# Kernel optimization log

Measured on AMD Instinct MI355X. Metric: run time of the kernel, lower is better.

The kernel has to match this reference:

```python
import jax, jax.numpy as jnp
import numpy as np

D_MODEL = 256
NUM_HEADS = 8
DIM_HEAD = D_MODEL // NUM_HEADS
EPS = 1e-6
MASK_BIAS = -1.0e9


def setup_inputs() -> dict:
    key = jax.random.key(0)
    ks = jax.random.split(key, 10)
    B, S = 2, 4096
    x = jax.random.normal(ks[0], (B, S, D_MODEL), dtype=jnp.float32)
    pad_mask = jnp.zeros((B, S), dtype=jnp.float32)  # 1.0 => padded position
    scale = 1.0 / np.sqrt(D_MODEL)
    Wq = jax.random.normal(ks[1], (D_MODEL, D_MODEL), dtype=jnp.float32) * scale
    bq = jnp.zeros((D_MODEL,), dtype=jnp.float32)
    Wk = jax.random.normal(ks[2], (D_MODEL, D_MODEL), dtype=jnp.float32) * scale
    bk = jnp.zeros((D_MODEL,), dtype=jnp.float32)
    Wv = jax.random.normal(ks[3], (D_MODEL, D_MODEL), dtype=jnp.float32) * scale
    bv = jnp.zeros((D_MODEL,), dtype=jnp.float32)
    gamma = jnp.ones((D_MODEL,), dtype=jnp.float32)
    beta = jnp.zeros((D_MODEL,), dtype=jnp.float32)
    return {"x": x, "pad_mask": pad_mask, "Wq": Wq, "bq": bq, "Wk": Wk,
            "bk": bk, "Wv": Wv, "bv": bv, "gamma": gamma, "beta": beta}


def _layer_norm(h, gamma, beta):
    mu = jnp.mean(h, axis=-1, keepdims=True)
    var = jnp.mean(jnp.square(h - mu), axis=-1, keepdims=True)
    return gamma * (h - mu) * jax.lax.rsqrt(var + EPS) + beta


def reference(x, pad_mask, Wq, bq, Wk, bk, Wv, bv, gamma, beta):
    B, S, D = x.shape
    q = x @ Wq + bq  # [B,S,D]
    k = x @ Wk + bk
    v = x @ Wv + bv
    # split heads: [B,S,D] -> [B,H,S,Dh]
    def split(t):
        return t.reshape(B, S, NUM_HEADS, DIM_HEAD).transpose(0, 2, 1, 3)
    qh, kh, vh = split(q), split(k), split(v)
    w = jnp.einsum("bhqd,bhkd->bhqk", qh, kh)  # [B,H,S,S]
    # faithful to source: mask added BEFORE the 1/sqrt(dim_head) scaling
    w = w + pad_mask[:, None, None, :] * MASK_BIAS
    w = w / jnp.sqrt(jnp.float32(DIM_HEAD))
    attn = jax.nn.softmax(w, axis=-1)
    # dropout is identity at inference
    out = jnp.einsum("bhqk,bhkd->bhqd", attn, vh)  # [B,H,S,Dh]
    out = out.transpose(0, 2, 1, 3).reshape(B, S, D)
    return _layer_norm(out + x, gamma, beta)
```

## Files before the change

kernel.cpp:

```cpp
#include <hip/hip_runtime.h>
#include <hip/hip_bf16.h>

#define D_MODEL 256
#define NUM_HEADS 8
#define DIM_HEAD 32
#define SEQ 4096
#define BATCH 2
#define NROWS (BATCH * SEQ)
#define LN_EPS 1e-6f
#define MASK_BIAS -1.0e9f
#define SCALE 0.17677669529663687f
#define LOG2E 1.4426950408889634f
#define QSCALE (SCALE * LOG2E)

typedef __attribute__((ext_vector_type(8))) short short8;
typedef __attribute__((ext_vector_type(4))) float f32x4;

static __device__ __forceinline__ unsigned short f2b(float f) {
    union { __hip_bfloat16 b; unsigned short u; } cv;
    cv.b = __float2bfloat16(f);
    return cv.u;
}
static __device__ __forceinline__ unsigned int pk_bf16(float lo, float hi) {
    union { __hip_bfloat162 v; unsigned int u; } cv;
    cv.v = __float22bfloat162_rn(make_float2(lo, hi));
    return cv.u;
}
static __device__ __forceinline__ float exp2_raw(float x) {
#if __has_builtin(__builtin_amdgcn_exp2f)
    return __builtin_amdgcn_exp2f(x);
#else
    float r;
    asm volatile("v_exp_f32 %0, %1" : "=v"(r) : "v"(x));
    return r;
#endif
}
static __device__ __forceinline__ void load_lds16(const void* g, void* l) {
    __builtin_amdgcn_global_load_lds(
        (const __attribute__((address_space(1))) unsigned int*)g,
        (__attribute__((address_space(3))) unsigned int*)l, 16, 0, 0);
}

__global__ __launch_bounds__(256) void prep_kernel(
    const float* __restrict__ Wq, const float* __restrict__ Wk,
    const float* __restrict__ Wv,
    const float* __restrict__ bq, const float* __restrict__ bk,
    const float* __restrict__ bv,
    const float* __restrict__ pad,
    unsigned short* __restrict__ Wt, float* __restrict__ biasc,
    float* __restrict__ T2)
{
    const int blk = blockIdx.x;
    const int t = threadIdx.x;
    if (blk < 48) {
        const int w = blk >> 4;
        const int k0 = (blk & 15) * 16;
        const float* W = (w == 0) ? Wq : (w == 1) ? Wk : Wv;
        float v[16];
        #pragma unroll
        for (int k = 0; k < 16; k++)
            v[k] = W[(size_t)(k0 + k) * 256 + t];
        unsigned int u[8];
        #pragma unroll
        for (int i = 0; i < 8; i++)
            u[i] = pk_bf16(v[2 * i], v[2 * i + 1]);
        unsigned short* dst = Wt + (size_t)(w * 256 + t) * 256 + k0;
        *(uint4*)(dst)     = make_uint4(u[0], u[1], u[2], u[3]);
        *(uint4*)(dst + 8) = make_uint4(u[4], u[5], u[6], u[7]);
        if ((blk & 15) == 0) {
            const float* bb = (w == 0) ? bq : (w == 1) ? bk : bv;
            biasc[w * 256 + t] = bb[t];
        }
    } else {
        const int i = (blk - 48) * 256 + t;
        T2[i] = pad[i] * (MASK_BIAS * SCALE * LOG2E);
    }
}

__global__ __launch_bounds__(256) void qkv_mfma_kernel(
    const float* __restrict__ x, const unsigned short* __restrict__ Wt,
    const float* __restrict__ biasc,
    unsigned short* __restrict__ Qh, unsigned short* __restrict__ Kh,
    unsigned short* __restrict__ Vt)
{
    __shared__ float LW[4][16][102];

    const int lane = threadIdx.x & 63;
    const int wid  = threadIdx.x >> 6;
    const int c    = lane & 15;
    const int quad = lane >> 4;

    const int r0 = (blockIdx.x >> 3) * 64 + wid * 16;
    const int n0 = (blockIdx.x & 7) * 96;

    f32x4 acc[6];
    float bias[6];
    #pragma unroll
    for (int t = 0; t < 6; t++) {
        acc[t] = (f32x4){0.f, 0.f, 0.f, 0.f};
        bias[t] = biasc[n0 + 16 * t + c];
    }

    const float* xp0 = x + (size_t)(r0 + c) * D_MODEL + quad * 8;
    const unsigned short* wp0 = Wt + (size_t)(n0 + c) * 256 + quad * 8;

    for (int k0 = 0; k0 < 256; k0 += 32) {
        const float4 a0 = *(const float4*)(xp0 + k0);
        const float4 a1 = *(const float4*)(xp0 + k0 + 4);
        union { unsigned int u[4]; short8 s; } af;
        af.u[0] = pk_bf16(a0.x, a0.y);
        af.u[1] = pk_bf16(a0.z, a0.w);
        af.u[2] = pk_bf16(a1.x, a1.y);
        af.u[3] = pk_bf16(a1.z, a1.w);
        #pragma unroll
        for (int t = 0; t < 6; t++) {
            const short8 bf = *(const short8*)(wp0 + (size_t)(16 * t) * 256 + k0);
            acc[t] = __builtin_amdgcn_mfma_f32_16x16x32_bf16(af.s, bf, acc[t], 0, 0, 0);
        }
    }

    float* lw = &LW[wid][0][0];
    #pragma unroll
    for (int t = 0; t < 6; t++) {
        const int col = n0 + 16 * t;
        const int mm  = col >> 8;
        float v0 = acc[t][0] + bias[t];
        float v1 = acc[t][1] + bias[t];
        float v2 = acc[t][2] + bias[t];
        float v3 = acc[t][3] + bias[t];
        if (mm == 2) {
            const int dim = (col & 255) + c;
            const int h = dim >> 5, d = dim & 31;
            const int row = r0 + quad * 4;
            const int bb = row >> 12;
            const int s  = row & (SEQ - 1);
            const size_t bh = (size_t)(bb * NUM_HEADS + h);
            uint2 pk = make_uint2(pk_bf16(v0, v1), pk_bf16(v2, v3));
            *(uint2*)(Vt + (bh * DIM_HEAD + d) * SEQ + s) = pk;
        } else {
            if (mm == 0) {
                v0 *= QSCALE; v1 *= QSCALE; v2 *= QSCALE; v3 *= QSCALE;
            }
            const int e = 16 * t + c;
            lw[(quad * 4 + 0) * 102 + e] = v0;
            lw[(quad * 4 + 1) * 102 + e] = v1;
            lw[(quad * 4 + 2) * 102 + e] = v2;
            lw[(quad * 4 + 3) * 102 + e] = v3;
        }
    }

    #pragma unroll
    for (int hg = 0; hg < 3; hg++) {
        const int col32 = n0 + 32 * hg;
        const int mm = col32 >> 8;
        if (mm == 2) continue;
        unsigned short* Pm = (mm == 0) ? Qh : Kh;
        const int h = (col32 & 255) >> 5;
        const int row = r0 + (lane & 15);
        const size_t bh = (size_t)((row >> 12) * NUM_HEADS + h);
        const int srow = row & (SEQ - 1);
        unsigned short* Pr = Pm + (bh * SEQ + srow) * DIM_HEAD;
        #pragma unroll
        for (int ii = 0; ii < 2; ii++) {
            const int cc = (lane >> 4) + 4 * ii;
            const int e = (lane & 15) * 102 + 32 * hg + cc * 4;
            const float2 lo = *(const float2*)&lw[e];
            const float2 hi = *(const float2*)&lw[e + 2];
            uint2 pk = make_uint2(pk_bf16(lo.x, lo.y), pk_bf16(hi.x, hi.y));
            *(uint2*)(Pr + cc * 4) = pk;
        }
    }
}

__global__ __launch_bounds__(512, 4) void attn_mfma_kernel(
    const unsigned short* __restrict__ Qh, const unsigned short* __restrict__ Kh,
    const unsigned short* __restrict__ Vt, const float* __restrict__ T2,
    float* __restrict__ O)
{
    __shared__ __align__(16) unsigned char smem[50688];
    unsigned short* smem_s = (unsigned short*)smem;
    float* Tf = (float*)(smem + 49152);

    const int lane = threadIdx.x & 63;
    const int wid  = threadIdx.x >> 6;
    const int cwid = wid & 3;
    const int shalf = wid >> 2;
    const int c    = lane & 15;
    const int quad = lane >> 4;

    const int gw = blockIdx.x;
    const int q0 = (gw & 31) * 128;
    const int h  = (gw >> 5) & (NUM_HEADS - 1);
    const int b  = gw >> 8;
    const size_t bh = (size_t)(b * NUM_HEADS + h);

    const int perm = ((c & 12) << 1) | (c & 3);

    const unsigned short* Kb = Kh + bh * SEQ * DIM_HEAD;
    const unsigned short* Vb = Vt + bh * DIM_HEAD * SEQ;
    const float* Tb = T2 + (size_t)b * SEQ;

    const int qrow = q0 + cwid * 32;
    const short8 qfA = *(const short8*)(Qh + (bh * SEQ + qrow + c) * DIM_HEAD + quad * 8);
    const short8 qfB = *(const short8*)(Qh + (bh * SEQ + qrow + 16 + c) * DIM_HEAD + quad * 8);

    union { unsigned int u[4]; short8 s; } ones;
    ones.u[0] = ones.u[1] = ones.u[2] = ones.u[3] = 0x3F803F80u;

    const int f0 = ((perm >> 1) ^ (perm >> 3)) & 3;
    const int f1 = (((perm + 4) >> 1) ^ ((perm + 4) >> 3)) & 3;
    const int kA = perm * 32 + ((quad ^ f0) << 3);
    const int kB = (perm + 4) * 32 + ((quad ^ f1) << 3);
    const int g0 = quad ^ (c & 7);
    const int vbase0 = c * 128 + (g0 << 3);
    const int vbase1 = (16 + c) * 128 + (g0 << 3);

    const int skey = (lane >> 2);
    const int sgK  = lane & 3;
    const int sdim = lane >> 4;
    const int sgV  = lane & 15;

    f32x4 oA0 = {0.f,0.f,0.f,0.f}, oA1 = {0.f,0.f,0.f,0.f};
    f32x4 oB0 = {0.f,0.f,0.f,0.f}, oB1 = {0.f,0.f,0.f,0.f};
    f32x4 laccA = {0.f,0.f,0.f,0.f}, laccB = {0.f,0.f,0.f,0.f};

    auto stage = [&](int ch, int pb) {
        const int s0 = ch * 128;
        if (wid < 4) {
            #pragma unroll
            for (int jj = 0; jj < 2; jj++) {
                const int j = wid * 2 + jj;
                const int key = j * 16 + skey;
                const int f = ((key >> 1) ^ (key >> 3)) & 3;
                load_lds16(Kb + (size_t)(s0 + key) * 32 + ((sgK ^ f) << 3),
                           &smem_s[pb * 4096 + j * 512]);
            }
        } else {
            #pragma unroll
            for (int jj = 0; jj < 2; jj++) {
                const int j = (wid - 4) * 2 + jj;
                const int dim = j * 4 + sdim;
                load_lds16(Vb + (size_t)dim * SEQ + s0 + ((sgV ^ (dim & 7)) << 3),
                           &smem_s[12288 + pb * 4096 + j * 512]);
            }
            if (wid == 7 && lane < 32)
                load_lds16(Tb + s0 + lane * 4, Tf + pb * 128);
        }
    };

    auto sub = [&](int pb, int s) {
        const short8 kf0 = *(const short8*)&smem_s[pb * 4096 + s * 1024 + kA];
        const short8 kf1 = *(const short8*)&smem_s[pb * 4096 + s * 1024 + kB];
        const short8 vf0 = *(const short8*)&smem_s[12288 + pb * 4096 + (vbase0 ^ (s << 5))];
        const short8 vf1 = *(const short8*)&smem_s[12288 + pb * 4096 + (vbase1 ^ (s << 5))];
        const f32x4 c0 = *(const f32x4*)&Tf[pb * 128 + s * 32 + quad * 8];
        const f32x4 c1 = *(const f32x4*)&Tf[pb * 128 + s * 32 + quad * 8 + 4];

        const f32x4 sA0 = __builtin_amdgcn_mfma_f32_16x16x32_bf16(kf0, qfA, c0, 0, 0, 0);
        const f32x4 sA1 = __builtin_amdgcn_mfma_f32_16x16x32_bf16(kf1, qfA, c1, 0, 0, 0);
        const f32x4 sB0 = __builtin_amdgcn_mfma_f32_16x16x32_bf16(kf0, qfB, c0, 0, 0, 0);
        const f32x4 sB1 = __builtin_amdgcn_mfma_f32_16x16x32_bf16(kf1, qfB, c1, 0, 0, 0);

        union { unsigned int u[4]; short8 s8; } pfA, pfB;
        {
            float p0 = exp2_raw(sA0[0]), p1 = exp2_raw(sA0[1]);
            float p2 = exp2_raw(sA0[2]), p3 = exp2_raw(sA0[3]);
            float p4 = exp2_raw(sA1[0]), p5 = exp2_raw(sA1[1]);
            float p6 = exp2_raw(sA1[2]), p7 = exp2_raw(sA1[3]);
            pfA.u[0] = pk_bf16(p0, p1);
            pfA.u[1] = pk_bf16(p2, p3);
            pfA.u[2] = pk_bf16(p4, p5);
            pfA.u[3] = pk_bf16(p6, p7);
        }
        {
            float p0 = exp2_raw(sB0[0]), p1 = exp2_raw(sB0[1]);
            float p2 = exp2_raw(sB0[2]), p3 = exp2_raw(sB0[3]);
            float p4 = exp2_raw(sB1[0]), p5 = exp2_raw(sB1[1]);
            float p6 = exp2_raw(sB1[2]), p7 = exp2_raw(sB1[3]);
            pfB.u[0] = pk_bf16(p0, p1);
            pfB.u[1] = pk_bf16(p2, p3);
            pfB.u[2] = pk_bf16(p4, p5);
            pfB.u[3] = pk_bf16(p6, p7);
        }

        laccA = __builtin_amdgcn_mfma_f32_16x16x32_bf16(ones.s, pfA.s8, laccA, 0, 0, 0);
        laccB = __builtin_amdgcn_mfma_f32_16x16x32_bf16(ones.s, pfB.s8, laccB, 0, 0, 0);
        oA0   = __builtin_amdgcn_mfma_f32_16x16x32_bf16(vf0,   pfA.s8, oA0,   0, 0, 0);
        oA1   = __builtin_amdgcn_mfma_f32_16x16x32_bf16(vf1,   pfA.s8, oA1,   0, 0, 0);
        oB0   = __builtin_amdgcn_mfma_f32_16x16x32_bf16(vf0,   pfB.s8, oB0,   0, 0, 0);
        oB1   = __builtin_amdgcn_mfma_f32_16x16x32_bf16(vf1,   pfB.s8, oB1,   0, 0, 0);
    };

    stage(0, 0);
    stage(1, 1);

    int rb = 0;
    int sb = 2;
    for (int ch = 0; ch < SEQ / 128; ++ch) {
        if (wid == 7)
            asm volatile("s_waitcnt vmcnt(3) lgkmcnt(0)" ::: "memory");
        else
            asm volatile("s_waitcnt vmcnt(2) lgkmcnt(0)" ::: "memory");
        __builtin_amdgcn_s_barrier();
        __builtin_amdgcn_sched_barrier(0);
        stage((ch + 2) & 31, sb);
        sub(rb, shalf * 2);
        sub(rb, shalf * 2 + 1);
        rb = (rb == 2) ? 0 : rb + 1;
        sb = (sb == 2) ? 0 : sb + 1;
    }

    asm volatile("s_waitcnt vmcnt(0) lgkmcnt(0)" ::: "memory");
    __builtin_amdgcn_s_barrier();

    float* CS = (float*)smem;
    if (wid >= 4) {
        const int slot = ((cwid * 64) + lane) * 20;
        *(f32x4*)&CS[slot + 0]  = oA0;
        *(f32x4*)&CS[slot + 4]  = oA1;
        *(f32x4*)&CS[slot + 8]  = oB0;
        *(f32x4*)&CS[slot + 12] = oB1;
        CS[slot + 16] = laccA[0];
        CS[slot + 17] = laccB[0];
    }
    asm volatile("s_waitcnt lgkmcnt(0)" ::: "memory");
    __builtin_amdgcn_s_barrier();
    if (wid < 4) {
        const int slot = ((cwid * 64) + lane) * 20;
        const f32x4 pA0 = *(const f32x4*)&CS[slot + 0];
        const f32x4 pA1 = *(const f32x4*)&CS[slot + 4];
        const f32x4 pB0 = *(const f32x4*)&CS[slot + 8];
        const f32x4 pB1 = *(const f32x4*)&CS[slot + 12];
        const float invA = 1.0f / (laccA[0] + CS[slot + 16]);
        const float invB = 1.0f / (laccB[0] + CS[slot + 17]);
        oA0 += pA0; oA1 += pA1; oB0 += pB0; oB1 += pB1;

        float* opA = O + ((size_t)(b * SEQ) + qrow + c) * D_MODEL + h * DIM_HEAD + quad * 4;
        float* opB = O + ((size_t)(b * SEQ) + qrow + 16 + c) * D_MODEL + h * DIM_HEAD + quad * 4;
        *(float4*)opA        = make_float4(oA0[0]*invA, oA0[1]*invA, oA0[2]*invA, oA0[3]*invA);
        *(float4*)(opA + 16) = make_float4(oA1[0]*invA, oA1[1]*invA, oA1[2]*invA, oA1[3]*invA);
        *(float4*)opB        = make_float4(oB0[0]*invB, oB0[1]*invB, oB0[2]*invB, oB0[3]*invB);
        *(float4*)(opB + 16) = make_float4(oB1[0]*invB, oB1[1]*invB, oB1[2]*invB, oB1[3]*invB);
    }
}

__global__ __launch_bounds__(256) void ln_kernel(
    float* AO,
    const float* __restrict__ x,
    const float* __restrict__ gamma, const float* __restrict__ beta)
{
    const int lane = threadIdx.x & 63;
    const int wid  = threadIdx.x >> 6;
    const size_t row = (size_t)blockIdx.x * 4 + wid;

    const float4 a  = ((const float4*)(AO + row * D_MODEL))[lane];
    const float4 xv = ((const float4*)(x + row * D_MODEL))[lane];
    float hv[4];
    hv[0] = a.x + xv.x;
    hv[1] = a.y + xv.y;
    hv[2] = a.z + xv.z;
    hv[3] = a.w + xv.w;

    float s = hv[0] + hv[1] + hv[2] + hv[3];
    #pragma unroll
    for (int off = 32; off > 0; off >>= 1) s += __shfl_xor(s, off, 64);
    const float mu = s * (1.0f / D_MODEL);

    float d0 = hv[0]-mu, d1 = hv[1]-mu, d2 = hv[2]-mu, d3 = hv[3]-mu;
    float ss = d0*d0 + d1*d1 + d2*d2 + d3*d3;
    #pragma unroll
    for (int off = 32; off > 0; off >>= 1) ss += __shfl_xor(ss, off, 64);
    const float rs = rsqrtf(ss * (1.0f / D_MODEL) + LN_EPS);

    const float4 g  = ((const float4*)gamma)[lane];
    const float4 bb = ((const float4*)beta)[lane];
    float4 y;
    y.x = g.x * d0 * rs + bb.x;
    y.y = g.y * d1 * rs + bb.y;
    y.z = g.z * d2 * rs + bb.z;
    y.w = g.w * d3 * rs + bb.w;
    ((float4*)(AO + row * D_MODEL))[lane] = y;
}

extern "C" void kernel_launch(void* const* d_in, const int* in_sizes, int n_in,
                              void* d_out, int out_size, void* d_ws, size_t ws_size,
                              hipStream_t stream)
{
    const float* x     = (const float*)d_in[0];
    const float* pad   = (const float*)d_in[1];
    const float* Wq    = (const float*)d_in[2];
    const float* bq    = (const float*)d_in[3];
    const float* Wk    = (const float*)d_in[4];
    const float* bk    = (const float*)d_in[5];
    const float* Wv    = (const float*)d_in[6];
    const float* bv    = (const float*)d_in[7];
    const float* gamma = (const float*)d_in[8];
    const float* beta  = (const float*)d_in[9];

    const size_t elems = (size_t)NROWS * D_MODEL;
    unsigned short* Qh = (unsigned short*)d_ws;
    unsigned short* Kh = Qh + elems;
    unsigned short* Vt = Kh + elems;
    float* T2 = (float*)(Vt + elems);
    unsigned short* Wt = (unsigned short*)(T2 + NROWS);
    float* biasc = (float*)(Wt + 768 * 256);
    float* AO = (float*)d_out;

    prep_kernel<<<80, 256, 0, stream>>>(Wq, Wk, Wv, bq, bk, bv, pad,
                                        Wt, biasc, T2);
    qkv_mfma_kernel<<<(NROWS / 64) * 8, 256, 0, stream>>>(x, Wt, biasc,
                                                          Qh, Kh, Vt);
    attn_mfma_kernel<<<BATCH * NUM_HEADS * (SEQ / 128), 512, 0, stream>>>(
        Qh, Kh, Vt, T2, AO);
    ln_kernel<<<NROWS / 4, 256, 0, stream>>>(AO, x, gamma, beta);
}
```

Measured before the change: 171.8 us.

## Software-pipeline PV MFMAs one chunk behind QK and exp computation

Splits the per-chunk attention step into a QK+exp stage and a PV accumulation stage. The PV MFMAs for the previous chunk are issued in the current iteration, using probabilities and V fragments held in registers. The aim is to overlap MFMA work with the exp2/packing VALU work and hide the dependency between exp and PV. The cost is extra register pressure from carrying eight short8 values across iterations, a prologue and an epilogue, and more sched_barriers.

```diff
diff --git a/kernel.cpp b/kernel.cpp
--- a/kernel.cpp
+++ b/kernel.cpp
@@ -224,6 +224,9 @@
     f32x4 oB0 = {0.f,0.f,0.f,0.f}, oB1 = {0.f,0.f,0.f,0.f};
     f32x4 laccA = {0.f,0.f,0.f,0.f}, laccB = {0.f,0.f,0.f,0.f};
 
+    short8 d_pfA0, d_pfB0, d_vf00, d_vf01;
+    short8 d_pfA1, d_pfB1, d_vf10, d_vf11;
+
     auto stage = [&](int ch, int pb) {
         const int s0 = ch * 128;
         if (wid < 4) {
@@ -248,11 +251,12 @@
         }
     };
 
-    auto sub = [&](int pb, int s) {
+    auto subQK = [&](int pb, int s, short8& o_pfA, short8& o_pfB,
+                     short8& o_vf0, short8& o_vf1) {
         const short8 kf0 = *(const short8*)&smem_s[pb * 4096 + s * 1024 + kA];
         const short8 kf1 = *(const short8*)&smem_s[pb * 4096 + s * 1024 + kB];
-        const short8 vf0 = *(const short8*)&smem_s[12288 + pb * 4096 + (vbase0 ^ (s << 5))];
-        const short8 vf1 = *(const short8*)&smem_s[12288 + pb * 4096 + (vbase1 ^ (s << 5))];
+        o_vf0 = *(const short8*)&smem_s[12288 + pb * 4096 + (vbase0 ^ (s << 5))];
+        o_vf1 = *(const short8*)&smem_s[12288 + pb * 4096 + (vbase1 ^ (s << 5))];
         const f32x4 c0 = *(const f32x4*)&Tf[pb * 128 + s * 32 + quad * 8];
         const f32x4 c1 = *(const f32x4*)&Tf[pb * 128 + s * 32 + quad * 8 + 4];
 
@@ -282,21 +286,42 @@
             pfB.u[2] = pk_bf16(p4, p5);
             pfB.u[3] = pk_bf16(p6, p7);
         }
-
-        laccA = __builtin_amdgcn_mfma_f32_16x16x32_bf16(ones.s, pfA.s8, laccA, 0, 0, 0);
-        laccB = __builtin_amdgcn_mfma_f32_16x16x32_bf16(ones.s, pfB.s8, laccB, 0, 0, 0);
-        oA0   = __builtin_amdgcn_mfma_f32_16x16x32_bf16(vf0,   pfA.s8, oA0,   0, 0, 0);
-        oA1   = __builtin_amdgcn_mfma_f32_16x16x32_bf16(vf1,   pfA.s8, oA1,   0, 0, 0);
-        oB0   = __builtin_amdgcn_mfma_f32_16x16x32_bf16(vf0,   pfB.s8, oB0,   0, 0, 0);
-        oB1   = __builtin_amdgcn_mfma_f32_16x16x32_bf16(vf1,   pfB.s8, oB1,   0, 0, 0);
+        o_pfA = pfA.s8;
+        o_pfB = pfB.s8;
+    };
+
+    auto PV = [&]() {
+        laccA = __builtin_amdgcn_mfma_f32_16x16x32_bf16(ones.s, d_pfA0, laccA, 0, 0, 0);
+        laccB = __builtin_amdgcn_mfma_f32_16x16x32_bf16(ones.s, d_pfB0, laccB, 0, 0, 0);
+        oA0   = __builtin_amdgcn_mfma_f32_16x16x32_bf16(d_vf00, d_pfA0, oA0,   0, 0, 0);
+        oA1   = __builtin_amdgcn_mfma_f32_16x16x32_bf16(d_vf01, d_pfA0, oA1,   0, 0, 0);
+        oB0   = __builtin_amdgcn_mfma_f32_16x16x32_bf16(d_vf00, d_pfB0, oB0,   0, 0, 0);
+        oB1   = __builtin_amdgcn_mfma_f32_16x16x32_bf16(d_vf01, d_pfB0, oB1,   0, 0, 0);
+        laccA = __builtin_amdgcn_mfma_f32_16x16x32_bf16(ones.s, d_pfA1, laccA, 0, 0, 0);
+        laccB = __builtin_amdgcn_mfma_f32_16x16x32_bf16(ones.s, d_pfB1, laccB, 0, 0, 0);
+        oA0   = __builtin_amdgcn_mfma_f32_16x16x32_bf16(d_vf10, d_pfA1, oA0,   0, 0, 0);
+        oA1   = __builtin_amdgcn_mfma_f32_16x16x32_bf16(d_vf11, d_pfA1, oA1,   0, 0, 0);
+        oB0   = __builtin_amdgcn_mfma_f32_16x16x32_bf16(d_vf10, d_pfB1, oB0,   0, 0, 0);
+        oB1   = __builtin_amdgcn_mfma_f32_16x16x32_bf16(d_vf11, d_pfB1, oB1,   0, 0, 0);
     };
 
     stage(0, 0);
     stage(1, 1);
 
-    int rb = 0;
-    int sb = 2;
-    for (int ch = 0; ch < SEQ / 128; ++ch) {
+    if (wid == 7)
+        asm volatile("s_waitcnt vmcnt(3) lgkmcnt(0)" ::: "memory");
+    else
+        asm volatile("s_waitcnt vmcnt(2) lgkmcnt(0)" ::: "memory");
+    __builtin_amdgcn_s_barrier();
+    __builtin_amdgcn_sched_barrier(0);
+    stage(2, 2);
+    __builtin_amdgcn_sched_barrier(0);
+    subQK(0, shalf * 2,     d_pfA0, d_pfB0, d_vf00, d_vf01);
+    subQK(0, shalf * 2 + 1, d_pfA1, d_pfB1, d_vf10, d_vf11);
+
+    int rb = 1;
+    int sb = 0;
+    for (int ch = 1; ch < SEQ / 128; ++ch) {
         if (wid == 7)
             asm volatile("s_waitcnt vmcnt(3) lgkmcnt(0)" ::: "memory");
         else
@@ -304,11 +329,14 @@
         __builtin_amdgcn_s_barrier();
         __builtin_amdgcn_sched_barrier(0);
         stage((ch + 2) & 31, sb);
-        sub(rb, shalf * 2);
-        sub(rb, shalf * 2 + 1);
+        __builtin_amdgcn_sched_barrier(0);
+        PV();
+        subQK(rb, shalf * 2,     d_pfA0, d_pfB0, d_vf00, d_vf01);
+        subQK(rb, shalf * 2 + 1, d_pfA1, d_pfB1, d_vf10, d_vf11);
         rb = (rb == 2) ? 0 : rb + 1;
         sb = (sb == 2) ? 0 : sb + 1;
     }
+    PV();
 
     asm volatile("s_waitcnt vmcnt(0) lgkmcnt(0)" ::: "memory");
     __builtin_amdgcn_s_barrier();
```

Result: no change. 171.2 us (-0.4%).
